# Performance work log

Hardware: AMD Instinct MI355X
Metric: run time of the kernel (lower is better)

## Reference

```python
import jax, jax.numpy as jnp
import numpy as np


def setup_inputs() -> dict:
    key = jax.random.key(0)
    ks = jax.random.split(key, 7)
    B, D, N, R = 256, 5120, 16, 160  # batch, d_inner, d_state, dt_rank
    x = jax.random.normal(ks[0], (B, D), jnp.float32)
    h0 = jax.random.normal(ks[1], (B, D, N), jnp.float32)
    W_x_dt = jax.random.normal(ks[2], (D, R), jnp.float32) * (1.0 / np.sqrt(D))
    W_dt = jax.random.normal(ks[3], (R, D), jnp.float32) * (1.0 / np.sqrt(R))
    b_dt = jax.random.normal(ks[4], (D,), jnp.float32)
    W_BC = jax.random.normal(ks[5], (D, 2 * N), jnp.float32) * (1.0 / np.sqrt(D))
    A_log = jax.random.normal(ks[6], (D, N), jnp.float32)
    return {"x": x, "h0": h0, "W_x_dt": W_x_dt, "W_dt": W_dt,
            "b_dt": b_dt, "W_BC": W_BC, "A_log": A_log}


def reference(x, h0, W_x_dt, W_dt, b_dt, W_BC, A_log):
    # Single-token Mamba selective SSM step (batch dims squeezed: x [B,D], h0 [B,D,N]).
    N = A_log.shape[1]
    # delta_t = softplus(dt_proj(delta_t_proj(x)))  -> [B, D]
    dt = jax.nn.softplus((x @ W_x_dt) @ W_dt + b_dt)
    # BC projection, split into B and C parts -> [B, N] each
    BC = x @ W_BC
    Bm, Cm = BC[:, :N], BC[:, N:]
    A = -jnp.exp(A_log)                              # [D, N]
    delta_A = jnp.exp(A[None, :, :] * dt[:, :, None])   # [B, D, N]
    delta_Bx = (dt * x)[:, :, None] * Bm[:, None, :]     # [B, D, N]
    h = delta_A * h0 + delta_Bx                          # new hidden state
    # y = h @ C (per-batch bmm over state dim) + x residual
    y = jnp.einsum('bdn,bn->bd', h, Cm) + x              # [B, D]
    return y
```

## Files before the change

### kernel.cpp

```cpp
#include <hip/hip_runtime.h>
#include <math.h>

#define BB 256
#define DD 5120
#define NN 16
#define RR 160
#define CT 192
#define NSPLIT 32
#define TMP_ELEMS (BB * CT)
#define NEGA_ELEMS (DD * NN)

__global__ __launch_bounds__(256) void k1_gemm(const float* __restrict__ x,
                                               const float* __restrict__ Wxdt,
                                               const float* __restrict__ Wbc,
                                               float* __restrict__ part) {
    __shared__ float xs[32][68];
    __shared__ float ws[32][64];
    const int tid = threadIdx.x;
    const int tx = tid & 15, ty = tid >> 4;
    const int c0 = blockIdx.x * 64;
    const int b0 = blockIdx.y * 64;
    const int k0 = blockIdx.z * 160;
    float acc[4][4] = {};

    for (int kc = 0; kc < 160; kc += 32) {
        {
            const int i  = tid >> 3;
            const int j4 = (tid & 7) * 4;
            #pragma unroll
            for (int rep = 0; rep < 2; ++rep) {
                const int row = i + rep * 32;
                const float4 v = *(const float4*)&x[(size_t)(b0 + row) * DD + k0 + kc + j4];
                xs[j4 + 0][row] = v.x;
                xs[j4 + 1][row] = v.y;
                xs[j4 + 2][row] = v.z;
                xs[j4 + 3][row] = v.w;
            }
        }
        {
            const int c4 = (tid & 15) * 4;
            const int r0 = tid >> 4;
            #pragma unroll
            for (int rep = 0; rep < 2; ++rep) {
                const int r  = r0 + rep * 16;
                const int kg = k0 + kc + r;
                const int cg = c0 + c4;
                float4 v;
                if (cg < RR) v = *(const float4*)&Wxdt[(size_t)kg * RR + cg];
                else         v = *(const float4*)&Wbc[(size_t)kg * 32 + (cg - RR)];
                *(float4*)&ws[r][c4] = v;
            }
        }
        __syncthreads();
        #pragma unroll
        for (int k = 0; k < 32; ++k) {
            const float4 a4 = *(const float4*)&xs[k][ty * 4];
            const float4 w4 = *(const float4*)&ws[k][tx * 4];
            const float av[4] = {a4.x, a4.y, a4.z, a4.w};
            const float wv[4] = {w4.x, w4.y, w4.z, w4.w};
            #pragma unroll
            for (int u = 0; u < 4; ++u)
                #pragma unroll
                for (int v = 0; v < 4; ++v)
                    acc[u][v] = fmaf(av[u], wv[v], acc[u][v]);
        }
        __syncthreads();
    }

    float* p = part + (size_t)blockIdx.z * TMP_ELEMS;
    #pragma unroll
    for (int u = 0; u < 4; ++u) {
        const int b = b0 + ty * 4 + u;
        *(float4*)&p[b * CT + c0 + tx * 4] =
            make_float4(acc[u][0], acc[u][1], acc[u][2], acc[u][3]);
    }
}

__global__ __launch_bounds__(256) void k_red(const float* __restrict__ part,
                                             const float* __restrict__ Alog,
                                             float* __restrict__ tmp,
                                             float* __restrict__ negA) {
    const int idx = blockIdx.x * 256 + threadIdx.x;
    if (idx < TMP_ELEMS) {
        float s = 0.f;
        #pragma unroll
        for (int z = 0; z < NSPLIT; ++z) s += part[(size_t)z * TMP_ELEMS + idx];
        tmp[idx] = s;
    } else {
        const int j = idx - TMP_ELEMS;
        negA[j] = -__expf(Alog[j]);
    }
}

__global__ __launch_bounds__(256) void k_dt(const float* __restrict__ tmp,
                                            const float* __restrict__ Wdt,
                                            const float* __restrict__ bdt,
                                            float* __restrict__ dtA) {
    __shared__ float ts[32][34];
    __shared__ float ws[32][64];
    const int tid = threadIdx.x;
    const int tx = tid & 15, ty = tid >> 4;
    const int d0 = blockIdx.x * 64;
    const int b0 = blockIdx.y * 32;

    float acc[2][4] = {};
    for (int kc = 0; kc < RR; kc += 32) {
        {
            const int row = tid >> 3;
            const int j4  = (tid & 7) * 4;
            const float4 v = *(const float4*)&tmp[(size_t)(b0 + row) * CT + kc + j4];
            ts[j4 + 0][row] = v.x;
            ts[j4 + 1][row] = v.y;
            ts[j4 + 2][row] = v.z;
            ts[j4 + 3][row] = v.w;
        }
        {
            const int c4 = (tid & 15) * 4;
            const int r0 = tid >> 4;
            #pragma unroll
            for (int rep = 0; rep < 2; ++rep) {
                const int r = r0 + rep * 16;
                *(float4*)&ws[r][c4] = *(const float4*)&Wdt[(size_t)(kc + r) * DD + d0 + c4];
            }
        }
        __syncthreads();
        #pragma unroll
        for (int k = 0; k < 32; ++k) {
            const float a0 = ts[k][ty * 2 + 0];
            const float a1 = ts[k][ty * 2 + 1];
            const float4 w4 = *(const float4*)&ws[k][tx * 4];
            const float wv[4] = {w4.x, w4.y, w4.z, w4.w};
            #pragma unroll
            for (int v = 0; v < 4; ++v) {
                acc[0][v] = fmaf(a0, wv[v], acc[0][v]);
                acc[1][v] = fmaf(a1, wv[v], acc[1][v]);
            }
        }
        __syncthreads();
    }

    const float4 bv = *(const float4*)&bdt[d0 + tx * 4];
    const float bb[4] = {bv.x, bv.y, bv.z, bv.w};
    #pragma unroll
    for (int u = 0; u < 2; ++u) {
        const int b = b0 + ty * 2 + u;
        float4 o;
        float* op = (float*)&o;
        #pragma unroll
        for (int v = 0; v < 4; ++v) {
            const float z = acc[u][v] + bb[v];
            op[v] = fmaxf(z, 0.f) + log1pf(__expf(-fabsf(z)));
        }
        *(float4*)&dtA[(size_t)b * DD + d0 + tx * 4] = o;
    }
}

__global__ __launch_bounds__(256) void k_epi(const float* __restrict__ x,
                                             const float* __restrict__ h0,
                                             const float* __restrict__ dtA,
                                             const float* __restrict__ negA,
                                             const float* __restrict__ tmp,
                                             float* __restrict__ out) {
    __shared__ float bc[32];
    const int tid = threadIdx.x;
    const int b  = blockIdx.y;
    const int d0 = blockIdx.x * 512;
    if (tid < 32) bc[tid] = tmp[(size_t)b * CT + RR + tid];
    __syncthreads();

    #pragma unroll
    for (int r = 0; r < 2; ++r) {
        const int d = d0 + r * 256 + tid;
        const size_t cell = (size_t)b * DD + d;
        const float dt  = dtA[cell];
        const float xe  = x[cell];
        const float dtx = dt * xe;
        const float* hp = &h0[cell * NN];
        const float* ap = &negA[(size_t)d * NN];
        float acc4[4] = {xe, 0.f, 0.f, 0.f};
        #pragma unroll
        for (int n4 = 0; n4 < NN; n4 += 4) {
            const float4 a4 = *(const float4*)&ap[n4];
            const float4 h4 = *(const float4*)&hp[n4];
            const float av[4] = {a4.x, a4.y, a4.z, a4.w};
            const float hv[4] = {h4.x, h4.y, h4.z, h4.w};
            #pragma unroll
            for (int q = 0; q < 4; ++q) {
                const int n = n4 + q;
                const float dA = __expf(av[q] * dt);
                const float h  = fmaf(dA, hv[q], dtx * bc[n]);
                acc4[q] = fmaf(h, bc[16 + n], acc4[q]);
            }
        }
        out[cell] = (acc4[0] + acc4[1]) + (acc4[2] + acc4[3]);
    }
}

extern "C" void kernel_launch(void* const* d_in, const int* in_sizes, int n_in,
                              void* d_out, int out_size, void* d_ws, size_t ws_size,
                              hipStream_t stream) {
    const float* x    = (const float*)d_in[0];
    const float* h0   = (const float*)d_in[1];
    const float* Wxdt = (const float*)d_in[2];
    const float* Wdt  = (const float*)d_in[3];
    const float* bdt  = (const float*)d_in[4];
    const float* Wbc  = (const float*)d_in[5];
    const float* Alog = (const float*)d_in[6];
    float* out = (float*)d_out;

    float* part = (float*)d_ws;
    float* tmp  = part + (size_t)NSPLIT * TMP_ELEMS;
    float* negA = tmp + TMP_ELEMS;
    float* dtA  = part;

    k1_gemm<<<dim3(3, 4, NSPLIT), 256, 0, stream>>>(x, Wxdt, Wbc, part);
    k_red<<<dim3((TMP_ELEMS + NEGA_ELEMS) / 256), 256, 0, stream>>>(part, Alog, tmp, negA);
    k_dt<<<dim3(DD / 64, BB / 32), 256, 0, stream>>>(tmp, Wdt, bdt, dtA);
    k_epi<<<dim3(DD / 512, BB), 256, 0, stream>>>(x, h0, dtA, negA, tmp, out);
}
```

Measured before the change: 184.0 us.

## Fuse dt projection GEMM into SSM epilogue kernel

```diff
diff --git a/kernel.cpp b/kernel.cpp
--- a/kernel.cpp
+++ b/kernel.cpp
@@ -92,104 +92,74 @@
     }
 }
 
-__global__ __launch_bounds__(256) void k_dt(const float* __restrict__ tmp,
-                                            const float* __restrict__ Wdt,
-                                            const float* __restrict__ bdt,
-                                            float* __restrict__ dtA) {
-    __shared__ float ts[32][34];
-    __shared__ float ws[32][64];
+__global__ __launch_bounds__(256) void k_fused(const float* __restrict__ x,
+                                               const float* __restrict__ h0,
+                                               const float* __restrict__ Wdt,
+                                               const float* __restrict__ bdt,
+                                               const float* __restrict__ tmp,
+                                               const float* __restrict__ negA,
+                                               float* __restrict__ out) {
     const int tid = threadIdx.x;
-    const int tx = tid & 15, ty = tid >> 4;
-    const int d0 = blockIdx.x * 64;
-    const int b0 = blockIdx.y * 32;
+    const int b0 = blockIdx.x * 4;
+    const int d0 = blockIdx.y * 256;
+    const int d  = d0 + tid;
+    const float* wcol = Wdt + d;
 
-    float acc[2][4] = {};
-    for (int kc = 0; kc < RR; kc += 32) {
-        {
-            const int row = tid >> 3;
-            const int j4  = (tid & 7) * 4;
-            const float4 v = *(const float4*)&tmp[(size_t)(b0 + row) * CT + kc + j4];
-            ts[j4 + 0][row] = v.x;
-            ts[j4 + 1][row] = v.y;
-            ts[j4 + 2][row] = v.z;
-            ts[j4 + 3][row] = v.w;
+    float acc[4] = {0.f, 0.f, 0.f, 0.f};
+    #pragma unroll 4
+    for (int k4 = 0; k4 < RR; k4 += 4) {
+        const float w0 = wcol[(size_t)(k4 + 0) * DD];
+        const float w1 = wcol[(size_t)(k4 + 1) * DD];
+        const float w2 = wcol[(size_t)(k4 + 2) * DD];
+        const float w3 = wcol[(size_t)(k4 + 3) * DD];
+        #pragma unroll
+        for (int bi = 0; bi < 4; ++bi) {
+            const float4 t4 = *(const float4*)&tmp[(size_t)(b0 + bi) * CT + k4];
+            acc[bi] = fmaf(t4.x, w0, acc[bi]);
+            acc[bi] = fmaf(t4.y, w1, acc[bi]);
+            acc[bi] = fmaf(t4.z, w2, acc[bi]);
+            acc[bi] = fmaf(t4.w, w3, acc[bi]);
         }
-        {
-            const int c4 = (tid & 15) * 4;
-            const int r0 = tid >> 4;
-            #pragma unroll
-            for (int rep = 0; rep < 2; ++rep) {
-                const int r = r0 + rep * 16;
-                *(float4*)&ws[r][c4] = *(const float4*)&Wdt[(size_t)(kc + r) * DD + d0 + c4];
-            }
-        }
-        __syncthreads();
-        #pragma unroll
-        for (int k = 0; k < 32; ++k) {
-            const float a0 = ts[k][ty * 2 + 0];
-            const float a1 = ts[k][ty * 2 + 1];
-            const float4 w4 = *(const float4*)&ws[k][tx * 4];
-            const float wv[4] = {w4.x, w4.y, w4.z, w4.w};
-            #pragma unroll
-            for (int v = 0; v < 4; ++v) {
-                acc[0][v] = fmaf(a0, wv[v], acc[0][v]);
-                acc[1][v] = fmaf(a1, wv[v], acc[1][v]);
-            }
-        }
-        __syncthreads();
     }
 
-    const float4 bv = *(const float4*)&bdt[d0 + tx * 4];
-    const float bb[4] = {bv.x, bv.y, bv.z, bv.w};
+    const float bdv = bdt[d];
+    float dtv[4];
     #pragma unroll
-    for (int u = 0; u < 2; ++u) {
-        const int b = b0 + ty * 2 + u;
-        float4 o;
-        float* op = (float*)&o;
+    for (int bi = 0; bi < 4; ++bi) {
+        const float z = acc[bi] + bdv;
+        dtv[bi] = fmaxf(z, 0.f) + log1pf(__expf(-fabsf(z)));
+    }
+
+    float av[16];
+    {
+        const float* ap = &negA[(size_t)d * NN];
         #pragma unroll
-        for (int v = 0; v < 4; ++v) {
-            const float z = acc[u][v] + bb[v];
-            op[v] = fmaxf(z, 0.f) + log1pf(__expf(-fabsf(z)));
+        for (int n4 = 0; n4 < NN; n4 += 4) {
+            const float4 a4 = *(const float4*)&ap[n4];
+            av[n4 + 0] = a4.x; av[n4 + 1] = a4.y;
+            av[n4 + 2] = a4.z; av[n4 + 3] = a4.w;
         }
-        *(float4*)&dtA[(size_t)b * DD + d0 + tx * 4] = o;
     }
-}
-
-__global__ __launch_bounds__(256) void k_epi(const float* __restrict__ x,
-                                             const float* __restrict__ h0,
-                                             const float* __restrict__ dtA,
-                                             const float* __restrict__ negA,
-                                             const float* __restrict__ tmp,
-                                             float* __restrict__ out) {
-    __shared__ float bc[32];
-    const int tid = threadIdx.x;
-    const int b  = blockIdx.y;
-    const int d0 = blockIdx.x * 512;
-    if (tid < 32) bc[tid] = tmp[(size_t)b * CT + RR + tid];
-    __syncthreads();
 
     #pragma unroll
-    for (int r = 0; r < 2; ++r) {
-        const int d = d0 + r * 256 + tid;
-        const size_t cell = (size_t)b * DD + d;
-        const float dt  = dtA[cell];
+    for (int bi = 0; bi < 4; ++bi) {
+        const size_t cell = (size_t)(b0 + bi) * DD + d;
+        const float dt  = dtv[bi];
         const float xe  = x[cell];
         const float dtx = dt * xe;
-        const float* hp = &h0[cell * NN];
-        const float* ap = &negA[(size_t)d * NN];
+        const float* hp  = &h0[cell * NN];
+        const float* bmp = &tmp[(size_t)(b0 + bi) * CT + RR];
         float acc4[4] = {xe, 0.f, 0.f, 0.f};
         #pragma unroll
         for (int n4 = 0; n4 < NN; n4 += 4) {
-            const float4 a4 = *(const float4*)&ap[n4];
             const float4 h4 = *(const float4*)&hp[n4];
-            const float av[4] = {a4.x, a4.y, a4.z, a4.w};
             const float hv[4] = {h4.x, h4.y, h4.z, h4.w};
             #pragma unroll
             for (int q = 0; q < 4; ++q) {
                 const int n = n4 + q;
-                const float dA = __expf(av[q] * dt);
-                const float h  = fmaf(dA, hv[q], dtx * bc[n]);
-                acc4[q] = fmaf(h, bc[16 + n], acc4[q]);
+                const float dA = __expf(av[n] * dt);
+                const float h  = fmaf(dA, hv[q], dtx * bmp[n]);
+                acc4[q] = fmaf(h, bmp[16 + n], acc4[q]);
             }
         }
         out[cell] = (acc4[0] + acc4[1]) + (acc4[2] + acc4[3]);
@@ -211,10 +181,8 @@
     float* part = (float*)d_ws;
     float* tmp  = part + (size_t)NSPLIT * TMP_ELEMS;
     float* negA = tmp + TMP_ELEMS;
-    float* dtA  = part;
 
     k1_gemm<<<dim3(3, 4, NSPLIT), 256, 0, stream>>>(x, Wxdt, Wbc, part);
     k_red<<<dim3((TMP_ELEMS + NEGA_ELEMS) / 256), 256, 0, stream>>>(part, Alog, tmp, negA);
-    k_dt<<<dim3(DD / 64, BB / 32), 256, 0, stream>>>(tmp, Wdt, bdt, dtA);
-    k_epi<<<dim3(DD / 512, BB), 256, 0, stream>>>(x, h0, dtA, negA, tmp, out);
+    k_fused<<<dim3(BB / 4, DD / 256), 256, 0, stream>>>(x, h0, Wdt, bdt, tmp, negA, out);
 }
```

Result: faster. 175.2 us (-4.8%).
